# Kernel optimization log

Measured on AMD Instinct MI355X. Metric: run time of the kernel, lower is better.

## Reference

```python
import jax, jax.numpy as jnp
import numpy as np

N_NODES = 50000
N_EDGES = 800000
D_IN = 128
HIDDEN = 128
N_GRAPHS = 512


def gcn_conv(x, W, b, src, dst, n):
    # PyG GCNConv: h = x @ W; add self loops; symmetric normalization deg^{-1/2}
    h = x @ W
    ones = jnp.ones(src.shape[0], dtype=h.dtype)
    deg = jax.ops.segment_sum(ones, dst, num_segments=n) + 1.0  # +1 for self loop
    dinv = jax.lax.rsqrt(deg)
    norm = dinv[src] * dinv[dst]                      # [E]
    msg = h[src] * norm[:, None]                      # gather + scale
    agg = jax.ops.segment_sum(msg, dst, num_segments=n)
    agg = agg + h * (dinv * dinv)[:, None]            # self-loop contribution
    return agg + b


def setup_inputs() -> dict:
    key = jax.random.key(0)
    ks = jax.random.split(key, 12)
    s = lambda fan_in: 1.0 / np.sqrt(fan_in)
    inp = {
        "x": jax.random.normal(ks[0], (N_NODES, D_IN), dtype=jnp.float32),
        "edge_index": jax.random.randint(ks[1], (2, N_EDGES), 0, N_NODES, dtype=jnp.int64),
        "batch": jnp.sort(jax.random.randint(ks[2], (N_NODES,), 0, N_GRAPHS, dtype=jnp.int64)),
        # conv 1
        "W1": jax.random.normal(ks[3], (D_IN, HIDDEN), dtype=jnp.float32) * s(D_IN),
        "b1": jnp.zeros((HIDDEN,), dtype=jnp.float32),
        # conv 2..n_layers SHARE these weights (Python list * replication)
        "W2": jax.random.normal(ks[4], (HIDDEN, HIDDEN), dtype=jnp.float32) * s(HIDDEN),
        "b2": jnp.zeros((HIDDEN,), dtype=jnp.float32),
        # MLP head
        "lw1": jax.random.normal(ks[5], (3 * HIDDEN, 3 * HIDDEN), dtype=jnp.float32) * s(3 * HIDDEN),
        "lb1": jnp.zeros((3 * HIDDEN,), dtype=jnp.float32),
        "lw2": jax.random.normal(ks[6], (3 * HIDDEN, HIDDEN), dtype=jnp.float32) * s(3 * HIDDEN),
        "lb2": jnp.zeros((HIDDEN,), dtype=jnp.float32),
        "lw3": jax.random.normal(ks[7], (HIDDEN, 1), dtype=jnp.float32) * s(HIDDEN),
        "lb3": jnp.zeros((1,), dtype=jnp.float32),
    }
    return inp


def reference(x, edge_index, batch, W1, b1, W2, b2, lw1, lb1, lw2, lb2, lw3, lb3):
    src, dst = edge_index[0], edge_index[1]
    n = x.shape[0]
    # n_layers = 3: conv1 (W1) -> relu, conv2 (W2) -> relu, conv3 (shared W2) -> relu
    h = jax.nn.relu(gcn_conv(x, W1, b1, src, dst, n))
    h = jax.nn.relu(gcn_conv(h, W2, b2, src, dst, n))
    h = jax.nn.relu(gcn_conv(h, W2, b2, src, dst, n))
    # tri-pool over graph ids
    ones = jnp.ones((n,), dtype=h.dtype)
    counts = jax.ops.segment_sum(ones, batch, num_segments=N_GRAPHS)  # [G]
    psum = jax.ops.segment_sum(h, batch, num_segments=N_GRAPHS)      # add pool
    pmean = psum / jnp.maximum(counts, 1.0)[:, None]
    pmax = jax.ops.segment_max(h, batch, num_segments=N_GRAPHS)
    pmax = jnp.where(counts[:, None] > 0, pmax, 0.0)
    g = jnp.concatenate([pmean, pmax, psum], axis=1)                 # [G, 3*H]
    # MLP head + sigmoid
    g = jax.nn.relu(g @ lw1 + lb1)
    g = jax.nn.relu(g @ lw2 + lb2)
    return jax.nn.sigmoid(g @ lw3 + lb3)                              # [G, 1]
```

## Files before the change

kernel.cpp:

```cpp
#include <hip/hip_runtime.h>
#include <hip/hip_bf16.h>
#include <hip/hip_fp16.h>
#include <math.h>


typedef _Float16 f16;
typedef _Float16 f16x2 __attribute__((ext_vector_type(2)));
typedef _Float16 f16x4 __attribute__((ext_vector_type(4)));
typedef _Float16 f16x8 __attribute__((ext_vector_type(8)));
typedef float f32x4 __attribute__((ext_vector_type(4)));

#define NR 8
#define NSPLIT 32
#define DSPLIT 16
#define QCAP 200000
#define BSZ_MAX 6272
#define QPAD 16
#define EPB 1024
#define ECAP 4096
#define SENTINEL 0xFFFFFFFFu

__device__ inline int wave_incl_scan(int v, int lane) {
    #pragma unroll
    for (int off = 1; off < 64; off <<= 1) {
        int nv = __shfl_up(v, off, 64);
        if (lane >= off) v += nv;
    }
    return v;
}

__global__ __launch_bounds__(256) void blk_reduce_fused(
    const int* __restrict__ deg, int n, int* __restrict__ bsum,
    float* __restrict__ dv) {
    __shared__ int ws[4];
    const int t = threadIdx.x;
    int i = blockIdx.x * 256 + t;
    int v = (i < n) ? deg[i] : 0;
    if (i < n) dv[i] = 1.0f / sqrtf((float)v + 1.0f);
    int r = v;
    #pragma unroll
    for (int off = 32; off > 0; off >>= 1) r += __shfl_down(r, off, 64);
    const int lane = t & 63, wid = t >> 6;
    if (lane == 0) ws[wid] = r;
    __syncthreads();
    if (t == 0) bsum[blockIdx.x] = ws[0] + ws[1] + ws[2] + ws[3];
}

__global__ __launch_bounds__(256) void scan_blocks(
    const int* __restrict__ in, int n, const int* __restrict__ bsum, int nb,
    int* __restrict__ out, int* __restrict__ out2) {
    __shared__ int ws[4];
    __shared__ int wpre[4];
    const int b = blockIdx.x, t = threadIdx.x;
    const int lane = t & 63, wid = t >> 6;

    int pv = 0;
    for (int j = t; j < b && j < nb; j += 256) pv += bsum[j];
    #pragma unroll
    for (int off = 32; off > 0; off >>= 1) pv += __shfl_down(pv, off, 64);
    if (lane == 0) ws[wid] = pv;
    __syncthreads();
    const int prefix = ws[0] + ws[1] + ws[2] + ws[3];

    const int i = b * 256 + t;
    int v = (i < n) ? in[i] : 0;
    int isc = wave_incl_scan(v, lane);
    if (lane == 63) wpre[wid] = isc;
    __syncthreads();
    int wb = 0;
    for (int w = 0; w < wid; ++w) wb += wpre[w];
    int ex = prefix + wb + isc - v;
    if (i < n) { out[i] = ex; out2[i] = ex; }
    if (i == n) out[n] = ex;
}

__global__ __launch_bounds__(256) void bucket_edges(
    const int* __restrict__ src, const int* __restrict__ dst, int E, int bsz,
    int N, int* __restrict__ deg, int* __restrict__ qcnt,
    unsigned* __restrict__ q) {
    __shared__ int lcnt[NR];
    __shared__ int lbase[NR];
    const int t = threadIdx.x;
    const int lane = t & 63;

    for (int i = blockIdx.x * 256 + t; i < N; i += gridDim.x * 256) deg[i] = 0;

    if (t < NR) lcnt[t] = 0;
    __syncthreads();

    const int e0 = blockIdx.x * EPB + t * 4;
    int  rj[4];
    int  lp[4];
    unsigned pk[4];
    if (e0 + 4 <= E) {
        int4 d4 = *(const int4*)(dst + e0);
        int4 s4 = *(const int4*)(src + e0);
        rj[0] = d4.x / bsz; pk[0] = ((unsigned)d4.x << 16) | (unsigned)s4.x;
        rj[1] = d4.y / bsz; pk[1] = ((unsigned)d4.y << 16) | (unsigned)s4.y;
        rj[2] = d4.z / bsz; pk[2] = ((unsigned)d4.z << 16) | (unsigned)s4.z;
        rj[3] = d4.w / bsz; pk[3] = ((unsigned)d4.w << 16) | (unsigned)s4.w;
    } else {
        #pragma unroll
        for (int j = 0; j < 4; ++j) {
            int e = e0 + j;
            if (e < E) {
                int d = dst[e];
                rj[j] = d / bsz;
                pk[j] = ((unsigned)d << 16) | (unsigned)src[e];
            } else rj[j] = -1;
        }
    }

    #pragma unroll
    for (int j = 0; j < 4; ++j) {
        #pragma unroll
        for (int rr = 0; rr < NR; ++rr) {
            bool mine = (rj[j] == rr);
            unsigned long long m = __ballot(mine);
            if (m) {
                int leader = __ffsll((long long)m) - 1;
                int base = 0;
                if (lane == leader) base = atomicAdd(&lcnt[rr], __popcll(m));
                base = __shfl(base, leader);
                if (mine) lp[j] = base + __popcll(m & ((1ull << lane) - 1ull));
            }
        }
    }
    __syncthreads();
    if (t < NR) {
        int padded = (lcnt[t] + 15) & ~15;
        lbase[t] = atomicAdd(&qcnt[t * QPAD], padded);
    }
    __syncthreads();
    #pragma unroll
    for (int j = 0; j < 4; ++j) {
        if (rj[j] >= 0) {
            int pos = lbase[rj[j]] + lp[j];
            if (pos < QCAP) q[(size_t)rj[j] * QCAP + pos] = pk[j];
        }
    }
    if (t < NR) {
        int base = lbase[t], c = lcnt[t], pad = (c + 15) & ~15;
        for (int i = c; i < pad; ++i)
            if (base + i < QCAP) q[(size_t)t * QCAP + base + i] = SENTINEL;
    }
}

__global__ __launch_bounds__(256) void deg_hist_split(
    const int* __restrict__ qcnt, const unsigned* __restrict__ q,
    int bsz, int N, int* __restrict__ deg) {
    __shared__ int hist[BSZ_MAX];
    const int r = blockIdx.x & (NR - 1);
    const int sp = blockIdx.x >> 3;
    const int lo = r * bsz;
    const int hi = min(lo + bsz, N);
    const int span = hi - lo;
    const int t = threadIdx.x;
    for (int i = t; i < span; i += 256) hist[i] = 0;
    __syncthreads();
    const int qn = min(qcnt[r * QPAD], QCAP);
    const int i0 = (int)((long long)qn * sp / DSPLIT);
    const int i1 = (int)((long long)qn * (sp + 1) / DSPLIT);
    const unsigned* qr = q + (size_t)r * QCAP;
    for (int i = i0 + t; i < i1; i += 256) {
        unsigned u = qr[i];
        if (u != SENTINEL) atomicAdd(&hist[(int)(u >> 16) - lo], 1);
    }
    __syncthreads();
    for (int i = t; i < span; i += 256) {
        int c = hist[i];
        if (c) atomicAdd(&deg[lo + i], c);
    }
}

__global__ __launch_bounds__(256) void fill_from_buckets(
    const int* __restrict__ qcnt, const unsigned* __restrict__ q,
    int* __restrict__ cursor, unsigned short* __restrict__ colsrc) {
    const int r = blockIdx.x & (NR - 1);
    const int sp = blockIdx.x >> 3;
    const int n = min(qcnt[r * QPAD], QCAP);
    const int i0 = (int)((long long)n * sp / NSPLIT);
    const int i1 = (int)((long long)n * (sp + 1) / NSPLIT);
    for (int i = i0 + threadIdx.x; i < i1; i += 256) {
        unsigned u = q[(size_t)r * QCAP + i];
        if (u == SENTINEL) continue;
        int d = u >> 16;
        int p = atomicAdd(&cursor[d], 1);
        colsrc[p] = (unsigned short)(u & 0xffffu);
    }
}

__global__ __launch_bounds__(256) void setup_misc(
    const float* __restrict__ W1, const float* __restrict__ W2,
    f16* __restrict__ Wt1, f16* __restrict__ Wt2,
    const int* __restrict__ batch, int N, int G, int* __restrict__ goff,
    int* __restrict__ qcnt) {
    const int b = blockIdx.x;
    if (b < 64) {
        if (b == 0 && threadIdx.x < NR * QPAD) qcnt[threadIdx.x] = 0;
        int idx = b * 256 + threadIdx.x;
        int n = idx >> 7, k = idx & 127;
        Wt1[idx] = (f16)W1[k * 128 + n];
        Wt2[idx] = (f16)W2[k * 128 + n];
    } else {
        int g = (b - 64) * 256 + threadIdx.x;
        if (g > G) return;
        int lo = 0, hi = N;
        while (lo < hi) {
            int mid = (lo + hi) >> 1;
            if (batch[mid] < g) lo = mid + 1; else hi = mid;
        }
        goff[g] = lo;
    }
}

template <bool F32IN>
__global__ __launch_bounds__(256) void gemm_mfma(
    const void* __restrict__ Ain, const f16* __restrict__ Wt,
    const float* __restrict__ dv, f16* __restrict__ out, int M) {
    const int lane = threadIdx.x & 63;
    const int w = threadIdx.x >> 6;
    const int wc = w & 1;
    const int wr = w >> 1;
    const int l15 = lane & 15;
    const int lg = lane >> 4;

    f16x8 wf[4][4];
    #pragma unroll
    for (int nt = 0; nt < 4; ++nt) {
        const f16* wp = Wt + (size_t)(wc * 64 + nt * 16 + l15) * 128 + lg * 8;
        #pragma unroll
        for (int kb = 0; kb < 4; ++kb)
            wf[nt][kb] = *(const f16x8*)(wp + kb * 32);
    }

    #pragma unroll
    for (int step = 0; step < 2; ++step) {
        const int m = blockIdx.x * 64 + step * 32 + wr * 16 + l15;
        const int mc = min(m, M - 1);
        f16x8 af[4];
        if constexpr (F32IN) {
            const float* ap = (const float*)Ain + (size_t)mc * 128 + lg * 8;
            #pragma unroll
            for (int kb = 0; kb < 4; ++kb) {
                float4 a = *(const float4*)(ap + kb * 32);
                float4 b = *(const float4*)(ap + kb * 32 + 4);
                f16x8 o;
                o[0] = (f16)a.x; o[1] = (f16)a.y; o[2] = (f16)a.z; o[3] = (f16)a.w;
                o[4] = (f16)b.x; o[5] = (f16)b.y; o[6] = (f16)b.z; o[7] = (f16)b.w;
                af[kb] = o;
            }
        } else {
            const f16* A = (const f16*)Ain;
            #pragma unroll
            for (int kb = 0; kb < 4; ++kb)
                af[kb] = *(const f16x8*)(A + ((size_t)kb * M + mc) * 32 + lg * 8);
        }
        const float d = dv[mc];
        #pragma unroll
        for (int nt = 0; nt < 4; ++nt) {
            f32x4 acc = {0.f, 0.f, 0.f, 0.f};
            #pragma unroll
            for (int kb = 0; kb < 4; ++kb)
                acc = __builtin_amdgcn_mfma_f32_16x16x32_f16(wf[nt][kb], af[kb], acc, 0, 0, 0);
            if (m < M) {
                f16x4 o;
                o[0] = (f16)(acc[0] * d);
                o[1] = (f16)(acc[1] * d);
                o[2] = (f16)(acc[2] * d);
                o[3] = (f16)(acc[3] * d);
                *(f16x4*)(out + ((size_t)(wc * 2 + (nt >> 1)) * M + m) * 32
                          + (nt & 1) * 16 + lg * 4) = o;
            }
        }
    }
}

__global__ __launch_bounds__(256) void agg_relu_b(
    const f16* __restrict__ hs, const float* __restrict__ dv,
    const float* __restrict__ bias, const int* __restrict__ rowoff,
    const unsigned short* __restrict__ colsrc, f16* __restrict__ out, int N) {
    __shared__ unsigned short ecache[ECAP];
    const int fb = blockIdx.x & 3;
    const int chunk = blockIdx.x >> 2;
    const int t = threadIdx.x;
    const int lane = t & 63;
    const int wav = t >> 6;
    const int sl = lane & 3;
    const int slot = lane >> 2;
    const int vb0 = chunk * 64;
    const int v = vb0 + wav * 16 + slot;

    const int vend = min(vb0 + 64, N);
    const int E0 = rowoff[vb0];
    const int E1 = rowoff[vend];
    const int nE = E1 - E0;
    const bool staged = (nE <= ECAP);
    if (staged) {
        for (int i = t; i < nE; i += 256) ecache[i] = colsrc[E0 + i];
    }
    __syncthreads();

    if (v >= N) return;

    const f16* slice = hs + (size_t)fb * N * 32;
    f16x8 h0 = *(const f16x8*)(slice + (size_t)v * 32 + sl * 8);
    float a0 = (float)h0[0], a1 = (float)h0[1], a2 = (float)h0[2], a3 = (float)h0[3];
    float a4 = (float)h0[4], a5 = (float)h0[5], a6 = (float)h0[6], a7 = (float)h0[7];

    const int e0 = rowoff[v], e1 = rowoff[v + 1];
    if (staged) {
        int eiter = e0 - E0;
        const int ee = e1 - E0;
        for (; eiter + 8 <= ee; eiter += 8) {
            int s[8];
            #pragma unroll
            for (int j = 0; j < 8; ++j) s[j] = ecache[eiter + j];
            f16x8 m[8];
            #pragma unroll
            for (int j = 0; j < 8; ++j)
                m[j] = *(const f16x8*)(slice + (size_t)s[j] * 32 + sl * 8);
            f16x8 t01 = m[0] + m[1];
            f16x8 t23 = m[2] + m[3];
            f16x8 t45 = m[4] + m[5];
            f16x8 t67 = m[6] + m[7];
            f16x8 tt = (t01 + t23) + (t45 + t67);
            a0 += (float)tt[0]; a1 += (float)tt[1];
            a2 += (float)tt[2]; a3 += (float)tt[3];
            a4 += (float)tt[4]; a5 += (float)tt[5];
            a6 += (float)tt[6]; a7 += (float)tt[7];
        }
        for (; eiter < ee; ++eiter) {
            int s = ecache[eiter];
            f16x8 mm = *(const f16x8*)(slice + (size_t)s * 32 + sl * 8);
            a0 += (float)mm[0]; a1 += (float)mm[1];
            a2 += (float)mm[2]; a3 += (float)mm[3];
            a4 += (float)mm[4]; a5 += (float)mm[5];
            a6 += (float)mm[6]; a7 += (float)mm[7];
        }
    } else {
        int e = e0;
        for (; e + 8 <= e1; e += 8) {
            int s[8];
            #pragma unroll
            for (int j = 0; j < 8; ++j) s[j] = colsrc[e + j];
            f16x8 m[8];
            #pragma unroll
            for (int j = 0; j < 8; ++j)
                m[j] = *(const f16x8*)(slice + (size_t)s[j] * 32 + sl * 8);
            f16x8 t01 = m[0] + m[1];
            f16x8 t23 = m[2] + m[3];
            f16x8 t45 = m[4] + m[5];
            f16x8 t67 = m[6] + m[7];
            f16x8 tt = (t01 + t23) + (t45 + t67);
            a0 += (float)tt[0]; a1 += (float)tt[1];
            a2 += (float)tt[2]; a3 += (float)tt[3];
            a4 += (float)tt[4]; a5 += (float)tt[5];
            a6 += (float)tt[6]; a7 += (float)tt[7];
        }
        for (; e < e1; ++e) {
            int s = colsrc[e];
            f16x8 mm = *(const f16x8*)(slice + (size_t)s * 32 + sl * 8);
            a0 += (float)mm[0]; a1 += (float)mm[1];
            a2 += (float)mm[2]; a3 += (float)mm[3];
            a4 += (float)mm[4]; a5 += (float)mm[5];
            a6 += (float)mm[6]; a7 += (float)mm[7];
        }
    }

    float d = dv[v];
    const float* bp = bias + fb * 32 + sl * 8;
    float4 b0 = *(const float4*)bp;
    float4 b1 = *(const float4*)(bp + 4);
    f16x8 o;
    o[0] = (f16)fmaxf(fmaf(d, a0, b0.x), 0.0f);
    o[1] = (f16)fmaxf(fmaf(d, a1, b0.y), 0.0f);
    o[2] = (f16)fmaxf(fmaf(d, a2, b0.z), 0.0f);
    o[3] = (f16)fmaxf(fmaf(d, a3, b0.w), 0.0f);
    o[4] = (f16)fmaxf(fmaf(d, a4, b1.x), 0.0f);
    o[5] = (f16)fmaxf(fmaf(d, a5, b1.y), 0.0f);
    o[6] = (f16)fmaxf(fmaf(d, a6, b1.z), 0.0f);
    o[7] = (f16)fmaxf(fmaf(d, a7, b1.w), 0.0f);
    *(f16x8*)(out + ((size_t)fb * N + v) * 32 + sl * 8) = o;
}

__global__ __launch_bounds__(384) void pool_mlp(
    const f16* __restrict__ h, const int* __restrict__ goff, int N,
    const float* __restrict__ lw1, const float* __restrict__ lb1,
    const float* __restrict__ lw2, const float* __restrict__ lb2,
    const float* __restrict__ lw3, const float* __restrict__ lb3,
    float* __restrict__ out) {
    __shared__ float psum[3][128];
    __shared__ float pmax[3][128];
    __shared__ float gin[384];
    __shared__ float h1[384];
    __shared__ float red[384];
    const int g = blockIdx.x, t = threadIdx.x;
    const int s = goff[g], e = goff[g + 1];

    {
        const int c = t >> 7, f = t & 127;
        const int fb = f >> 5, off = f & 31;
        const f16* slice = h + ((size_t)fb * N) * 32 + off;
        float sum = 0.0f, mx = 0.0f;
        for (int v = s + c; v < e; v += 3) {
            float val = (float)slice[(size_t)v * 32];
            sum += val;
            mx = fmaxf(mx, val);
        }
        psum[c][f] = sum;
        pmax[c][f] = mx;
    }
    __syncthreads();
    if (t < 128) {
        float ts = psum[0][t] + psum[1][t] + psum[2][t];
        float tm = fmaxf(fmaxf(pmax[0][t], pmax[1][t]), pmax[2][t]);
        float cnt = (float)(e - s);
        gin[t]       = ts / fmaxf(cnt, 1.0f);
        gin[128 + t] = tm;
        gin[256 + t] = ts;
    }
    __syncthreads();

    {
        const float* wp = lw1 + t;
        float a0 = 0.f, a1 = 0.f, a2 = 0.f, a3 = 0.f;
        for (int i = 0; i < 384; i += 4) {
            a0 = fmaf(gin[i],     wp[(size_t)i * 384],        a0);
            a1 = fmaf(gin[i + 1], wp[(size_t)(i + 1) * 384],  a1);
            a2 = fmaf(gin[i + 2], wp[(size_t)(i + 2) * 384],  a2);
            a3 = fmaf(gin[i + 3], wp[(size_t)(i + 3) * 384],  a3);
        }
        h1[t] = fmaxf(lb1[t] + (a0 + a1) + (a2 + a3), 0.0f);
    }
    __syncthreads();

    {
        const int jj = t & 127, chunk = t >> 7;
        const float* wp = lw2 + (size_t)chunk * 128 * 128 + jj;
        const float* hp = h1 + chunk * 128;
        float a0 = 0.f, a1 = 0.f, a2 = 0.f, a3 = 0.f;
        for (int i = 0; i < 128; i += 4) {
            a0 = fmaf(hp[i],     wp[(size_t)i * 128],       a0);
            a1 = fmaf(hp[i + 1], wp[(size_t)(i + 1) * 128], a1);
            a2 = fmaf(hp[i + 2], wp[(size_t)(i + 2) * 128], a2);
            a3 = fmaf(hp[i + 3], wp[(size_t)(i + 3) * 128], a3);
        }
        red[t] = (a0 + a1) + (a2 + a3);
    }
    __syncthreads();

    if (t < 128) {
        float h2 = fmaxf(lb2[t] + red[t] + red[t + 128] + red[t + 256], 0.0f);
        red[t] = h2 * lw3[t];
    }
    __syncthreads();
    if (t < 64) {
        float sv = red[t] + red[t + 64];
        #pragma unroll
        for (int off = 32; off > 0; off >>= 1) sv += __shfl_down(sv, off, 64);
        if (t == 0) out[g] = 1.0f / (1.0f + expf(-(sv + lb3[0])));
    }
}

extern "C" void kernel_launch(void* const* d_in, const int* in_sizes, int n_in,
                              void* d_out, int out_size, void* d_ws, size_t ws_size,
                              hipStream_t stream) {
    (void)n_in; (void)ws_size;
    const float* x     = (const float*)d_in[0];
    const int*   ei    = (const int*)d_in[1];
    const int*   batch = (const int*)d_in[2];
    const float* W1  = (const float*)d_in[3];
    const float* b1  = (const float*)d_in[4];
    const float* W2  = (const float*)d_in[5];
    const float* b2  = (const float*)d_in[6];
    const float* lw1 = (const float*)d_in[7];
    const float* lb1 = (const float*)d_in[8];
    const float* lw2 = (const float*)d_in[9];
    const float* lb2 = (const float*)d_in[10];
    const float* lw3 = (const float*)d_in[11];
    const float* lb3 = (const float*)d_in[12];
    float* out = (float*)d_out;

    const int N = in_sizes[2];
    const int E = in_sizes[1] / 2;
    const int G = out_size;

    const int* src = ei;
    const int* dst = ei + E;

    size_t off = 0;
    auto alloc = [&](size_t bytes) -> void* {
        void* p = (char*)d_ws + off;
        off += (bytes + 255) & ~(size_t)255;
        return p;
    };
    const int nb = (N + 255) / 256;

    f16*   hs     = (f16*)alloc((size_t)N * 128 * 2);
    f16*   hb     = (f16*)alloc((size_t)N * 128 * 2);
    f16*   Wt1    = (f16*)alloc((size_t)128 * 128 * 2);
    f16*   Wt2    = (f16*)alloc((size_t)128 * 128 * 2);
    float* dv     = (float*)alloc((size_t)N * 4);
    int*   deg    = (int*)alloc((size_t)N * 4);
    int*   rowoff = (int*)alloc((size_t)(N + 1) * 4);
    int*   cursor = (int*)alloc((size_t)N * 4);
    int*   bsum   = (int*)alloc((size_t)nb * 4);
    unsigned short* colsrc = (unsigned short*)alloc((size_t)E * 2);
    unsigned* q   = (unsigned*)alloc((size_t)NR * QCAP * 4);
    int*   qcnt   = (int*)alloc((size_t)NR * QPAD * 4);
    int*   goff   = (int*)alloc((size_t)(G + 1) * 4);

    const int nscan = (N + 1 + 255) / 256;
    const int bsz = (N + NR - 1) / NR;
    const int setup_blocks = 64 + (G + 1 + 255) / 256;

    setup_misc<<<setup_blocks, 256, 0, stream>>>(W1, W2, Wt1, Wt2, batch, N, G, goff, qcnt);
    bucket_edges<<<(E + EPB - 1) / EPB, 256, 0, stream>>>(src, dst, E, bsz, N, deg, qcnt, q);
    deg_hist_split<<<NR * DSPLIT, 256, 0, stream>>>(qcnt, q, bsz, N, deg);
    blk_reduce_fused<<<nb, 256, 0, stream>>>(deg, N, bsum, dv);
    scan_blocks<<<nscan, 256, 0, stream>>>(deg, N, bsum, nb, rowoff, cursor);
    fill_from_buckets<<<NR * NSPLIT, 256, 0, stream>>>(qcnt, q, cursor, colsrc);

    const int gemm_blocks = (N + 63) / 64;
    const int agg_blocks  = 4 * ((N + 63) / 64);

    gemm_mfma<true><<<gemm_blocks, 256, 0, stream>>>(x, Wt1, dv, hs, N);
    agg_relu_b<<<agg_blocks, 256, 0, stream>>>(hs, dv, b1, rowoff, colsrc, hb, N);
    gemm_mfma<false><<<gemm_blocks, 256, 0, stream>>>(hb, Wt2, dv, hs, N);
    agg_relu_b<<<agg_blocks, 256, 0, stream>>>(hs, dv, b2, rowoff, colsrc, hb, N);
    gemm_mfma<false><<<gemm_blocks, 256, 0, stream>>>(hb, Wt2, dv, hs, N);
    agg_relu_b<<<agg_blocks, 256, 0, stream>>>(hs, dv, b2, rowoff, colsrc, hb, N);

    pool_mlp<<<G, 384, 0, stream>>>(hb, goff, N, lw1, lb1, lw2, lb2, lw3, lb3, out);
}
```

Baseline: 238.3 us.

## Fuse degree reduce and scan into per-range scan using bucket totals

Removes the block-reduce and block-scan kernels. deg_hist_split now also counts the non-sentinel edges per destination range and atomically adds that total into rtot. A new 8-block, 1024-thread range_scan kernel then scans each range sequentially, starting from the prefix of rtot, and writes rowoff, cursor and dv. This saves one launch and the quadratic bsum prefix reads, but each block serially walks about 6250 elements with three barriers per 1024-element chunk, so parallelism is low.

```diff
diff --git a/kernel.cpp b/kernel.cpp
--- a/kernel.cpp
+++ b/kernel.cpp
@@ -27,51 +27,6 @@
         if (lane >= off) v += nv;
     }
     return v;
-}
-
-__global__ __launch_bounds__(256) void blk_reduce_fused(
-    const int* __restrict__ deg, int n, int* __restrict__ bsum,
-    float* __restrict__ dv) {
-    __shared__ int ws[4];
-    const int t = threadIdx.x;
-    int i = blockIdx.x * 256 + t;
-    int v = (i < n) ? deg[i] : 0;
-    if (i < n) dv[i] = 1.0f / sqrtf((float)v + 1.0f);
-    int r = v;
-    #pragma unroll
-    for (int off = 32; off > 0; off >>= 1) r += __shfl_down(r, off, 64);
-    const int lane = t & 63, wid = t >> 6;
-    if (lane == 0) ws[wid] = r;
-    __syncthreads();
-    if (t == 0) bsum[blockIdx.x] = ws[0] + ws[1] + ws[2] + ws[3];
-}
-
-__global__ __launch_bounds__(256) void scan_blocks(
-    const int* __restrict__ in, int n, const int* __restrict__ bsum, int nb,
-    int* __restrict__ out, int* __restrict__ out2) {
-    __shared__ int ws[4];
-    __shared__ int wpre[4];
-    const int b = blockIdx.x, t = threadIdx.x;
-    const int lane = t & 63, wid = t >> 6;
-
-    int pv = 0;
-    for (int j = t; j < b && j < nb; j += 256) pv += bsum[j];
-    #pragma unroll
-    for (int off = 32; off > 0; off >>= 1) pv += __shfl_down(pv, off, 64);
-    if (lane == 0) ws[wid] = pv;
-    __syncthreads();
-    const int prefix = ws[0] + ws[1] + ws[2] + ws[3];
-
-    const int i = b * 256 + t;
-    int v = (i < n) ? in[i] : 0;
-    int isc = wave_incl_scan(v, lane);
-    if (lane == 63) wpre[wid] = isc;
-    __syncthreads();
-    int wb = 0;
-    for (int w = 0; w < wid; ++w) wb += wpre[w];
-    int ex = prefix + wb + isc - v;
-    if (i < n) { out[i] = ex; out2[i] = ex; }
-    if (i == n) out[n] = ex;
 }
 
 __global__ __launch_bounds__(256) void bucket_edges(
@@ -148,29 +103,80 @@
 
 __global__ __launch_bounds__(256) void deg_hist_split(
     const int* __restrict__ qcnt, const unsigned* __restrict__ q,
-    int bsz, int N, int* __restrict__ deg) {
+    int bsz, int N, int* __restrict__ deg, int* __restrict__ rtot) {
     __shared__ int hist[BSZ_MAX];
+    __shared__ int csum[4];
     const int r = blockIdx.x & (NR - 1);
     const int sp = blockIdx.x >> 3;
     const int lo = r * bsz;
     const int hi = min(lo + bsz, N);
     const int span = hi - lo;
     const int t = threadIdx.x;
+    const int lane = t & 63, wid = t >> 6;
     for (int i = t; i < span; i += 256) hist[i] = 0;
     __syncthreads();
     const int qn = min(qcnt[r * QPAD], QCAP);
     const int i0 = (int)((long long)qn * sp / DSPLIT);
     const int i1 = (int)((long long)qn * (sp + 1) / DSPLIT);
     const unsigned* qr = q + (size_t)r * QCAP;
+    int cnt = 0;
     for (int i = i0 + t; i < i1; i += 256) {
         unsigned u = qr[i];
-        if (u != SENTINEL) atomicAdd(&hist[(int)(u >> 16) - lo], 1);
+        if (u != SENTINEL) {
+            atomicAdd(&hist[(int)(u >> 16) - lo], 1);
+            ++cnt;
+        }
     }
     __syncthreads();
     for (int i = t; i < span; i += 256) {
         int c = hist[i];
         if (c) atomicAdd(&deg[lo + i], c);
     }
+    #pragma unroll
+    for (int off = 32; off > 0; off >>= 1) cnt += __shfl_down(cnt, off, 64);
+    if (lane == 0) csum[wid] = cnt;
+    __syncthreads();
+    if (t == 0) atomicAdd(&rtot[r], csum[0] + csum[1] + csum[2] + csum[3]);
+}
+
+__global__ __launch_bounds__(1024) void range_scan(
+    const int* __restrict__ deg, const int* __restrict__ rtot,
+    int bsz, int N, int* __restrict__ rowoff, int* __restrict__ cursor,
+    float* __restrict__ dv) {
+    __shared__ int wsum[16];
+    __shared__ int carry_s;
+    const int r = blockIdx.x;
+    const int lo = r * bsz;
+    const int hi = min(lo + bsz, N);
+    const int t = threadIdx.x;
+    const int lane = t & 63, wid = t >> 6;
+
+    if (t == 0) {
+        int base = 0;
+        for (int j = 0; j < r; ++j) base += rtot[j];
+        carry_s = base;
+    }
+    __syncthreads();
+
+    for (int i0 = lo; i0 < hi; i0 += 1024) {
+        int i = i0 + t;
+        int v = (i < hi) ? deg[i] : 0;
+        if (i < hi) dv[i] = 1.0f / sqrtf((float)v + 1.0f);
+        int isc = wave_incl_scan(v, lane);
+        if (lane == 63) wsum[wid] = isc;
+        __syncthreads();
+        int carry = carry_s;
+        int wb = 0;
+        for (int w = 0; w < wid; ++w) wb += wsum[w];
+        int tot = 0;
+        for (int w = 0; w < 16; ++w) tot += wsum[w];
+        int ex = carry + wb + isc - v;
+        if (i < hi) { rowoff[i] = ex; cursor[i] = ex; }
+        __syncthreads();
+        if (t == 0) carry_s = carry + tot;
+        __syncthreads();
+    }
+    if (r == NR - 1 && t == 0) rowoff[N] = carry_s;
 }
 
 __global__ __launch_bounds__(256) void fill_from_buckets(
@@ -197,7 +203,7 @@
     int* __restrict__ qcnt) {
     const int b = blockIdx.x;
     if (b < 64) {
-        if (b == 0 && threadIdx.x < NR * QPAD) qcnt[threadIdx.x] = 0;
+        if (b == 0 && threadIdx.x < NR * QPAD + NR) qcnt[threadIdx.x] = 0;
         int idx = b * 256 + threadIdx.x;
         int n = idx >> 7, k = idx & 127;
         Wt1[idx] = (f16)W1[k * 128 + n];
@@ -495,7 +501,6 @@
         off += (bytes + 255) & ~(size_t)255;
         return p;
     };
-    const int nb = (N + 255) / 256;
 
     f16*   hs     = (f16*)alloc((size_t)N * 128 * 2);
     f16*   hb     = (f16*)alloc((size_t)N * 128 * 2);
@@ -505,21 +510,19 @@
     int*   deg    = (int*)alloc((size_t)N * 4);
     int*   rowoff = (int*)alloc((size_t)(N + 1) * 4);
     int*   cursor = (int*)alloc((size_t)N * 4);
-    int*   bsum   = (int*)alloc((size_t)nb * 4);
     unsigned short* colsrc = (unsigned short*)alloc((size_t)E * 2);
     unsigned* q   = (unsigned*)alloc((size_t)NR * QCAP * 4);
-    int*   qcnt   = (int*)alloc((size_t)NR * QPAD * 4);
+    int*   qcnt   = (int*)alloc((size_t)(NR * QPAD + NR) * 4);
     int*   goff   = (int*)alloc((size_t)(G + 1) * 4);
-
-    const int nscan = (N + 1 + 255) / 256;
+    int*   rtot   = qcnt + NR * QPAD;
+
     const int bsz = (N + NR - 1) / NR;
     const int setup_blocks = 64 + (G + 1 + 255) / 256;
 
     setup_misc<<<setup_blocks, 256, 0, stream>>>(W1, W2, Wt1, Wt2, batch, N, G, goff, qcnt);
     bucket_edges<<<(E + EPB - 1) / EPB, 256, 0, stream>>>(src, dst, E, bsz, N, deg, qcnt, q);
-    deg_hist_split<<<NR * DSPLIT, 256, 0, stream>>>(qcnt, q, bsz, N, deg);
-    blk_reduce_fused<<<nb, 256, 0, stream>>>(deg, N, bsum, dv);
-    scan_blocks<<<nscan, 256, 0, stream>>>(deg, N, bsum, nb, rowoff, cursor);
+    deg_hist_split<<<NR * DSPLIT, 256, 0, stream>>>(qcnt, q, bsz, N, deg, rtot);
+    range_scan<<<NR, 1024, 0, stream>>>(deg, rtot, bsz, N, rowoff, cursor, dv);
     fill_from_buckets<<<NR * NSPLIT, 256, 0, stream>>>(qcnt, q, cursor, colsrc);
 
     const int gemm_blocks = (N + 63) / 64;
```

After: 245.8 us. 1.03x slower.
